# Kernel tuning notes

Hardware: AMD Instinct MI355X
Metric: run time of the kernel (lower is better)

## Reference

```python
import jax, jax.numpy as jnp
import numpy as np

N_NODES = 10000
EPS = 1e-5


def _layernorm(x, gamma, beta):
    mu = jnp.mean(x, axis=-1, keepdims=True)
    var = jnp.mean(jnp.square(x - mu), axis=-1, keepdims=True)
    return (x - mu) * jax.lax.rsqrt(var + EPS) * gamma + beta


def _sage_pool_layer(h, src, dst, Wp, bp, Ws, Wn, b, gamma, beta):
    # DGL SAGEConv(aggregator='pool'):
    #   m_u = relu(h_u @ Wp^T + bp); h_neigh[v] = max_{u in N(v)} m_u (0 if no neighbors)
    #   rst = h @ Ws^T + h_neigh @ Wn^T + b
    m = jax.nn.relu(h @ Wp.T + bp)              # [N, d]
    msg = m[src]                                 # [E, d] gather
    agg = jax.ops.segment_max(msg, dst, num_segments=N_NODES)
    agg = jnp.where(jnp.isfinite(agg), agg, 0.0)  # isolated nodes -> 0
    rst = h @ Ws.T + agg @ Wn.T + b
    # gsage_layer: LayerNorm, then Encoder applies relu (dropout inactive in eval)
    return jax.nn.relu(_layernorm(rst, gamma, beta))


def setup_inputs() -> dict:
    key = jax.random.key(0)
    ks = jax.random.split(key, 16)
    d = 256
    E = 320000
    s = 1.0 / np.sqrt(d)
    inp = {
        "h": jax.random.normal(ks[0], (N_NODES, d), dtype=jnp.float32),
        "edge_src": jax.random.randint(ks[1], (E,), 0, N_NODES, dtype=jnp.int32),
        "edge_dst": jax.random.randint(ks[2], (E,), 0, N_NODES, dtype=jnp.int32),
    }
    for li in range(2):
        kk = jax.random.split(ks[3 + li], 3)
        inp[f"Wp{li}"] = jax.random.normal(kk[0], (d, d), dtype=jnp.float32) * s
        inp[f"bp{li}"] = jnp.zeros((d,), jnp.float32)
        inp[f"Ws{li}"] = jax.random.normal(kk[1], (d, d), dtype=jnp.float32) * s
        inp[f"Wn{li}"] = jax.random.normal(kk[2], (d, d), dtype=jnp.float32) * s
        inp[f"b{li}"] = jnp.zeros((d,), jnp.float32)
        inp[f"g{li}"] = jnp.ones((d,), jnp.float32)
        inp[f"be{li}"] = jnp.zeros((d,), jnp.float32)
    return inp


def reference(h, edge_src, edge_dst,
              Wp0, bp0, Ws0, Wn0, b0, g0, be0,
              Wp1, bp1, Ws1, Wn1, b1, g1, be1):
    h = _sage_pool_layer(h, edge_src, edge_dst, Wp0, bp0, Ws0, Wn0, b0, g0, be0)
    h = _sage_pool_layer(h, edge_src, edge_dst, Wp1, bp1, Ws1, Wn1, b1, g1, be1)
    return h
```

## Files before the change

kernel.cpp:

```cpp
#include <hip/hip_runtime.h>

#define D 256
#define CAP 128
#define ASTRIDE 280
#define LN_EPS 1e-5f

typedef short short8 __attribute__((ext_vector_type(8)));
typedef float floatx4 __attribute__((ext_vector_type(4)));
typedef unsigned short u16x4 __attribute__((ext_vector_type(4)));

typedef const __attribute__((address_space(1))) void* gas_t;
typedef __attribute__((address_space(3))) void* las_t;

#define WAIT_VM(n) __builtin_amdgcn_s_waitcnt(((n) & 0xF) | (((n) >> 4) << 14) | (7 << 4) | (0xF << 8))

__device__ __forceinline__ u16x4 umax4(u16x4 a, u16x4 b) {
#if __has_builtin(__builtin_elementwise_max)
    return __builtin_elementwise_max(a, b);
#else
    u16x4 r;
    r.x = a.x > b.x ? a.x : b.x; r.y = a.y > b.y ? a.y : b.y;
    r.z = a.z > b.z ? a.z : b.z; r.w = a.w > b.w ? a.w : b.w;
    return r;
#endif
}

__device__ __forceinline__ unsigned short f2b(float f) {
    union { float f; unsigned int u; } x; x.f = f;
    unsigned int u = x.u + 0x7FFFu + ((x.u >> 16) & 1u);
    return (unsigned short)(u >> 16);
}

#define GEMM_HALF(APTR_EXPR, WPTR, K0H)                                         \
    {                                                                           \
        short8 aF[4], bF[4][4];                                                 \
        _Pragma("unroll") for (int ks = 0; ks < 4; ks++)                        \
            aF[ks] = APTR_EXPR(K0H + ks * 32);                                  \
        _Pragma("unroll") for (int ks = 0; ks < 4; ks++)                        \
        _Pragma("unroll") for (int t = 0; t < 4; t++)                           \
            bF[ks][t] = *(const short8*)((WPTR) + t * 16 * D + (K0H) + ks * 32);\
        _Pragma("unroll") for (int ks = 0; ks < 4; ks++) {                      \
            acc[0] = __builtin_amdgcn_mfma_f32_16x16x32_bf16(aF[ks], bF[ks][0], acc[0], 0, 0, 0); \
            acc[1] = __builtin_amdgcn_mfma_f32_16x16x32_bf16(aF[ks], bF[ks][1], acc[1], 0, 0, 0); \
            acc[2] = __builtin_amdgcn_mfma_f32_16x16x32_bf16(aF[ks], bF[ks][2], acc[2], 0, 0, 0); \
            acc[3] = __builtin_amdgcn_mfma_f32_16x16x32_bf16(aF[ks], bF[ks][3], acc[3], 0, 0, 0); \
        }                                                                       \
    }

__global__ __launch_bounds__(256) void prep_kernel(
    const float* __restrict__ w0, const float* __restrict__ w1,
    const float* __restrict__ w2, const float* __restrict__ w3,
    const float* __restrict__ w4, const float* __restrict__ w5,
    unsigned short* __restrict__ wb,
    const float* __restrict__ h, unsigned short* __restrict__ hb, int nh4,
    int* __restrict__ cnt, unsigned short* __restrict__ mb, int N)
{
    const int blk = blockIdx.x;
    const int tid = threadIdx.x;
    if (blk < 384) {
        const int wsel = blk >> 6;
        const float* src;
        switch (wsel) {
            case 0: src = w0; break; case 1: src = w1; break;
            case 2: src = w2; break; case 3: src = w3; break;
            case 4: src = w4; break; default: src = w5; break;
        }
        const int idx = (blk & 63) * 1024 + tid * 4;
        const float4 v = *(const float4*)(src + idx);
        ushort4 o;
        o.x = f2b(v.x); o.y = f2b(v.y); o.z = f2b(v.z); o.w = f2b(v.w);
        *(ushort4*)(wb + (size_t)wsel * 65536 + idx) = o;
    } else if (blk < 1024) {
        int i = (blk - 384) * 256 + tid;
        const int stride = 640 * 256;
        for (; i < nh4; i += stride) {
            const float4 v = *(const float4*)(h + (size_t)i * 4);
            ushort4 o;
            o.x = f2b(v.x); o.y = f2b(v.y); o.z = f2b(v.z); o.w = f2b(v.w);
            *(ushort4*)(hb + (size_t)i * 4) = o;
        }
    } else if (blk < 1064) {
        const int i = (blk - 1024) * 256 + tid;
        if (i < N) cnt[i] = 0;
    } else {
        mb[(size_t)N * D + tid] = 0;
    }
}

__global__ __launch_bounds__(64, 4) void gemm_relu(
    const unsigned short* __restrict__ A, const unsigned short* __restrict__ W,
    const float* __restrict__ bias, unsigned short* __restrict__ out_b, int N,
    const int* __restrict__ esrc, const int* __restrict__ edst,
    int* __restrict__ cnt, unsigned short* __restrict__ csr, int E, int ngemm)
{
    if ((int)blockIdx.x >= ngemm) {
        const int nsb = gridDim.x - ngemm;
        int i = ((int)blockIdx.x - ngemm) * 64 + threadIdx.x;
        const int stride = nsb * 64;
        for (; i < E; i += stride) {
            const int d = edst[i];
            const int pos = atomicAdd(&cnt[d], 1);
            if (pos < CAP) csr[(size_t)d * CAP + pos] = (unsigned short)esrc[i];
        }
        return;
    }

    const int lane = threadIdx.x;
    const int quad = lane >> 4;
    const int l16 = lane & 15;
    const int blk = blockIdx.x;
    const int row0 = (blk >> 2) * 16;
    const int col0 = (blk & 3) * 64;
    const int koff = quad * 8;

    floatx4 acc[4];
#pragma unroll
    for (int t = 0; t < 4; t++) acc[t] = (floatx4)(0.f);

    const unsigned short* aptr = A + (size_t)(row0 + l16) * D + koff;
    const unsigned short* wptr = W + (size_t)(col0 + l16) * D + koff;
#define A_GLOBAL(K) (*(const short8*)(aptr + (K)))
    GEMM_HALF(A_GLOBAL, wptr, 0)
    GEMM_HALF(A_GLOBAL, wptr, 128)
#undef A_GLOBAL

#pragma unroll
    for (int t = 0; t < 4; t++) {
        const float bcol = bias[col0 + t * 16 + l16];
#pragma unroll
        for (int r = 0; r < 4; r++) {
            const int rg = row0 + quad * 4 + r;
            const int col = col0 + t * 16 + l16;
            out_b[(size_t)rg * D + col] = f2b(fmaxf(acc[t][r] + bcol, 0.f));
        }
    }
}

__global__ __launch_bounds__(256, 3) void gemm_ln_pool(
    const unsigned short* __restrict__ A, const unsigned short* __restrict__ Wself,
    const unsigned short* __restrict__ Wneigh,
    const unsigned short* __restrict__ mpool,
    const int* __restrict__ cnt, const unsigned short* __restrict__ csr,
    const float* __restrict__ bias,
    const float* __restrict__ gamma, const float* __restrict__ beta,
    unsigned short* __restrict__ out_b, float* __restrict__ out_f, int N)
{
    __shared__ unsigned short idxS[16][CAP];
    __shared__ unsigned short gbuf[4][2][8][D];
    __shared__ unsigned short aggS[16 * ASTRIDE];
    __shared__ float redS[4][16], redS2[4][16], muA[16], rsA[16];

    const int tid = threadIdx.x;
    const int wave = tid >> 6;
    const int lane = tid & 63;
    const int quad = lane >> 4;
    const int l16 = lane & 15;
    const int row0 = blockIdx.x * 16;
    const int koff = quad * 8;
    const int rbase = wave * 4;
    const int half = lane >> 5;
    const int l32 = lane & 31;

    int degs[4];
#pragma unroll
    for (int rr = 0; rr < 4; rr++) degs[rr] = min(cnt[row0 + rbase + rr], CAP);
    int P = max(max(degs[0], degs[1]), max(degs[2], degs[3]));
    const int P2 = (P + 1) & ~1;
#pragma unroll
    for (int rr = 0; rr < 4; rr++) {
        const int rg = row0 + rbase + rr;
        for (int i = lane; i < P2; i += 64)
            idxS[rbase + rr][i] = (i < degs[rr]) ? csr[(size_t)rg * CAP + i]
                                                 : (unsigned short)N;
    }

    floatx4 acc[4];
#pragma unroll
    for (int t = 0; t < 4; t++) acc[t] = (floatx4)(0.f);

    {
        const unsigned short* aptr = A + (size_t)(row0 + l16) * D + koff;
        const unsigned short* wptr = Wself + (size_t)(wave * 64 + l16) * D + koff;
#pragma unroll
        for (int k0 = 0; k0 < D; k0 += 32) {
            const short8 av = *(const short8*)(aptr + k0);
            const short8 b0 = *(const short8*)(wptr + k0);
            const short8 b1 = *(const short8*)(wptr + 16 * D + k0);
            const short8 b2 = *(const short8*)(wptr + 32 * D + k0);
            const short8 b3 = *(const short8*)(wptr + 48 * D + k0);
            acc[0] = __builtin_amdgcn_mfma_f32_16x16x32_bf16(av, b0, acc[0], 0, 0, 0);
            acc[1] = __builtin_amdgcn_mfma_f32_16x16x32_bf16(av, b1, acc[1], 0, 0, 0);
            acc[2] = __builtin_amdgcn_mfma_f32_16x16x32_bf16(av, b2, acc[2], 0, 0, 0);
            acc[3] = __builtin_amdgcn_mfma_f32_16x16x32_bf16(av, b3, acc[3], 0, 0, 0);
        }
    }

    {
        const int nb = P2 >> 1;
        u16x4 mx[4];
#pragma unroll
        for (int rr = 0; rr < 4; rr++) mx[rr] = (u16x4)(0);

#define ISSUE_BURST(bi, buf)                                                    \
        {                                                                       \
            _Pragma("unroll") for (int rr = 0; rr < 4; rr++) {                  \
                const int jj = idxS[rbase + rr][2 * (bi) + half];               \
                const unsigned short* g = mpool + (size_t)jj * D + l32 * 8;     \
                __builtin_amdgcn_global_load_lds(                               \
                    (gas_t)g, (las_t)&gbuf[wave][buf][rr * 2][0], 16, 0, 0);    \
            }                                                                   \
        }

        if (nb > 0) ISSUE_BURST(0, 0);
        if (nb > 1) ISSUE_BURST(1, 1);
        for (int b = 0; b < nb; b++) {
            if (b + 1 < nb) WAIT_VM(4); else WAIT_VM(0);
            const int buf = b & 1;
#pragma unroll
            for (int rr = 0; rr < 4; rr++) {
                const u16x4 a0 = *(const u16x4*)&gbuf[wave][buf][rr * 2 + 0][lane * 4];
                const u16x4 a1 = *(const u16x4*)&gbuf[wave][buf][rr * 2 + 1][lane * 4];
                mx[rr] = umax4(mx[rr], umax4(a0, a1));
            }
            if (b + 2 < nb) ISSUE_BURST(b + 2, buf);
        }
#undef ISSUE_BURST
#pragma unroll
        for (int rr = 0; rr < 4; rr++)
            *(u16x4*)&aggS[(rbase + rr) * ASTRIDE + lane * 4] = mx[rr];
    }
    __syncthreads();

    {
        const unsigned short* wptr = Wneigh + (size_t)(wave * 64 + l16) * D + koff;
#pragma unroll
        for (int k0 = 0; k0 < D; k0 += 32) {
            const short8 av = *(const short8*)&aggS[l16 * ASTRIDE + koff + k0];
            const short8 b0 = *(const short8*)(wptr + k0);
            const short8 b1 = *(const short8*)(wptr + 16 * D + k0);
            const short8 b2 = *(const short8*)(wptr + 32 * D + k0);
            const short8 b3 = *(const short8*)(wptr + 48 * D + k0);
            acc[0] = __builtin_amdgcn_mfma_f32_16x16x32_bf16(av, b0, acc[0], 0, 0, 0);
            acc[1] = __builtin_amdgcn_mfma_f32_16x16x32_bf16(av, b1, acc[1], 0, 0, 0);
            acc[2] = __builtin_amdgcn_mfma_f32_16x16x32_bf16(av, b2, acc[2], 0, 0, 0);
            acc[3] = __builtin_amdgcn_mfma_f32_16x16x32_bf16(av, b3, acc[3], 0, 0, 0);
        }
    }

    float bcol[4];
#pragma unroll
    for (int t = 0; t < 4; t++) bcol[t] = bias[wave * 64 + t * 16 + l16];
#pragma unroll
    for (int t = 0; t < 4; t++)
#pragma unroll
        for (int r = 0; r < 4; r++) acc[t][r] += bcol[t];

#pragma unroll
    for (int r = 0; r < 4; r++) {
        float s = 0.f, s2 = 0.f;
#pragma unroll
        for (int t = 0; t < 4; t++) {
            const float v = acc[t][r];
            s += v; s2 += v * v;
        }
        s += __shfl_xor(s, 1);  s2 += __shfl_xor(s2, 1);
        s += __shfl_xor(s, 2);  s2 += __shfl_xor(s2, 2);
        s += __shfl_xor(s, 4);  s2 += __shfl_xor(s2, 4);
        s += __shfl_xor(s, 8);  s2 += __shfl_xor(s2, 8);
        if (l16 == 0) {
            redS[wave][quad * 4 + r] = s;
            redS2[wave][quad * 4 + r] = s2;
        }
    }
    __syncthreads();
    if (tid < 16) {
        const float S  = redS[0][tid] + redS[1][tid] + redS[2][tid] + redS[3][tid];
        const float S2 = redS2[0][tid] + redS2[1][tid] + redS2[2][tid] + redS2[3][tid];
        const float mu = S * (1.f / D);
        float var = S2 * (1.f / D) - mu * mu;
        var = fmaxf(var, 0.f);
        muA[tid] = mu;
        rsA[tid] = rsqrtf(var + LN_EPS);
    }
    __syncthreads();

    float gcol[4], becol[4];
#pragma unroll
    for (int t = 0; t < 4; t++) {
        gcol[t] = gamma[wave * 64 + t * 16 + l16];
        becol[t] = beta[wave * 64 + t * 16 + l16];
    }
#pragma unroll
    for (int r = 0; r < 4; r++) {
        const int rl = quad * 4 + r;
        const int rg = row0 + rl;
        const float mu = muA[rl];
        const float rs = rsA[rl];
#pragma unroll
        for (int t = 0; t < 4; t++) {
            const int col = wave * 64 + t * 16 + l16;
            float o = (acc[t][r] - mu) * rs * gcol[t] + becol[t];
            o = fmaxf(o, 0.f);
            if (out_f) out_f[(size_t)rg * D + col] = o;
            else       out_b[(size_t)rg * D + col] = f2b(o);
        }
    }
}

extern "C" void kernel_launch(void* const* d_in, const int* in_sizes, int n_in,
                              void* d_out, int out_size, void* d_ws, size_t ws_size,
                              hipStream_t stream) {
    const float* h    = (const float*)d_in[0];
    const int*   esrc = (const int*)d_in[1];
    const int*   edst = (const int*)d_in[2];
    const float* Wp0  = (const float*)d_in[3];
    const float* bp0  = (const float*)d_in[4];
    const float* Ws0  = (const float*)d_in[5];
    const float* Wn0  = (const float*)d_in[6];
    const float* b0   = (const float*)d_in[7];
    const float* g0   = (const float*)d_in[8];
    const float* be0  = (const float*)d_in[9];
    const float* Wp1  = (const float*)d_in[10];
    const float* bp1  = (const float*)d_in[11];
    const float* Ws1  = (const float*)d_in[12];
    const float* Wn1  = (const float*)d_in[13];
    const float* b1   = (const float*)d_in[14];
    const float* g1   = (const float*)d_in[15];
    const float* be1  = (const float*)d_in[16];

    const int N = in_sizes[0] / D;
    const int E = in_sizes[1];
    const size_t ND = (size_t)N * D;

    unsigned short* hb  = (unsigned short*)d_ws;
    unsigned short* mb  = hb + ND;
    unsigned short* h1b = mb + ND + D;
    unsigned short* wb  = h1b + ND;
    int* cnt = (int*)(wb + 6 * 65536);
    unsigned short* csr = (unsigned short*)(cnt + N);

    unsigned short* wpb0 = wb + 0 * 65536;
    unsigned short* wsb0 = wb + 1 * 65536;
    unsigned short* wnb0 = wb + 2 * 65536;
    unsigned short* wpb1 = wb + 3 * 65536;
    unsigned short* wsb1 = wb + 4 * 65536;
    unsigned short* wnb1 = wb + 5 * 65536;

    const int rblocks = (N / 16) * 4;
    const int pblocks = N / 16;
    const int sblocks = 1024;

    prep_kernel<<<1065, 256, 0, stream>>>(Wp0, Ws0, Wn0, Wp1, Ws1, Wn1, wb,
                                          h, hb, (int)(ND / 4), cnt, mb, N);

    gemm_relu<<<rblocks + sblocks, 64, 0, stream>>>(hb, wpb0, bp0, mb, N,
                                                    esrc, edst, cnt, csr, E, rblocks);
    gemm_ln_pool<<<pblocks, 256, 0, stream>>>(hb, wsb0, wnb0, mb, cnt, csr,
                                              b0, g0, be0, h1b, nullptr, N);

    gemm_relu<<<rblocks, 64, 0, stream>>>(h1b, wpb1, bp1, mb, N,
                                          esrc, edst, cnt, csr, 0, rblocks);
    gemm_ln_pool<<<pblocks, 256, 0, stream>>>(h1b, wsb1, wnb1, mb, cnt, csr,
                                              b1, g1, be1, nullptr, (float*)d_out, N);
}
```

Measured before the change: 216.1 us.

## Fuse fp32-to-bf16 input conversion into layer-0 GEMM loads and regroup row blocks

Drops the separate pass that converted the fp32 node features to bf16 in the prep kernel. The layer-0 GEMMs now read fp32 rows directly and convert them to bf16 in registers. The gemm_relu block index is also remapped so groups of 8 row tiles share their 4 column tiles, which should improve L2 reuse of A rows. This removes one full write-and-read of the feature matrix, but layer 0 now reads twice as many bytes for A in both GEMMs and adds a runtime branch on the A source.

New measurement: 217.5 us. Within noise of the previous version (+0.6%).

```diff
diff --git a/kernel.cpp b/kernel.cpp
--- a/kernel.cpp
+++ b/kernel.cpp
@@ -31,11 +31,22 @@
     return (unsigned short)(u >> 16);
 }
 
-#define GEMM_HALF(APTR_EXPR, WPTR, K0H)                                         \
+__device__ __forceinline__ short8 ldA_f32(const float* p) {
+    const float4 a = *(const float4*)p;
+    const float4 b = *(const float4*)(p + 4);
+    short8 r;
+    r[0] = (short)f2b(a.x); r[1] = (short)f2b(a.y);
+    r[2] = (short)f2b(a.z); r[3] = (short)f2b(a.w);
+    r[4] = (short)f2b(b.x); r[5] = (short)f2b(b.y);
+    r[6] = (short)f2b(b.z); r[7] = (short)f2b(b.w);
+    return r;
+}
+
+#define GEMM_HALF(A_EXPR, WPTR, K0H)                                            \
     {                                                                           \
         short8 aF[4], bF[4][4];                                                 \
         _Pragma("unroll") for (int ks = 0; ks < 4; ks++)                        \
-            aF[ks] = APTR_EXPR(K0H + ks * 32);                                  \
+            aF[ks] = A_EXPR(K0H + ks * 32);                                     \
         _Pragma("unroll") for (int ks = 0; ks < 4; ks++)                        \
         _Pragma("unroll") for (int t = 0; t < 4; t++)                           \
             bF[ks][t] = *(const short8*)((WPTR) + t * 16 * D + (K0H) + ks * 32);\
@@ -52,7 +63,6 @@
     const float* __restrict__ w2, const float* __restrict__ w3,
     const float* __restrict__ w4, const float* __restrict__ w5,
     unsigned short* __restrict__ wb,
-    const float* __restrict__ h, unsigned short* __restrict__ hb, int nh4,
     int* __restrict__ cnt, unsigned short* __restrict__ mb, int N)
 {
     const int blk = blockIdx.x;
@@ -70,17 +80,8 @@
         ushort4 o;
         o.x = f2b(v.x); o.y = f2b(v.y); o.z = f2b(v.z); o.w = f2b(v.w);
         *(ushort4*)(wb + (size_t)wsel * 65536 + idx) = o;
-    } else if (blk < 1024) {
-        int i = (blk - 384) * 256 + tid;
-        const int stride = 640 * 256;
-        for (; i < nh4; i += stride) {
-            const float4 v = *(const float4*)(h + (size_t)i * 4);
-            ushort4 o;
-            o.x = f2b(v.x); o.y = f2b(v.y); o.z = f2b(v.z); o.w = f2b(v.w);
-            *(ushort4*)(hb + (size_t)i * 4) = o;
-        }
-    } else if (blk < 1064) {
-        const int i = (blk - 1024) * 256 + tid;
+    } else if (blk < 424) {
+        const int i = (blk - 384) * 256 + tid;
         if (i < N) cnt[i] = 0;
     } else {
         mb[(size_t)N * D + tid] = 0;
@@ -88,8 +89,9 @@
 }
 
 __global__ __launch_bounds__(64, 4) void gemm_relu(
-    const unsigned short* __restrict__ A, const unsigned short* __restrict__ W,
-    const float* __restrict__ bias, unsigned short* __restrict__ out_b, int N,
+    const float* __restrict__ Af, const unsigned short* __restrict__ Ab,
+    const unsigned short* __restrict__ W,
+    const float* __restrict__ bias, unsigned short* __restrict__ out_b, int nrow,
     const int* __restrict__ esrc, const int* __restrict__ edst,
     int* __restrict__ cnt, unsigned short* __restrict__ csr, int E, int ngemm)
 {
@@ -105,39 +107,47 @@
         return;
     }
 
+    const int blk = blockIdx.x;
+    const int g = blk >> 5;
+    const int o = blk & 31;
+    const int c = o >> 3;
+    const int r = g * 8 + (o & 7);
+    if (r >= nrow) return;
+
     const int lane = threadIdx.x;
     const int quad = lane >> 4;
     const int l16 = lane & 15;
-    const int blk = blockIdx.x;
-    const int row0 = (blk >> 2) * 16;
-    const int col0 = (blk & 3) * 64;
+    const int row0 = r * 16;
+    const int col0 = c * 64;
     const int koff = quad * 8;
 
     floatx4 acc[4];
 #pragma unroll
     for (int t = 0; t < 4; t++) acc[t] = (floatx4)(0.f);
 
-    const unsigned short* aptr = A + (size_t)(row0 + l16) * D + koff;
+    const unsigned short* aptr = Ab ? Ab + (size_t)(row0 + l16) * D + koff : nullptr;
+    const float*          afp  = Af ? Af + (size_t)(row0 + l16) * D + koff : nullptr;
     const unsigned short* wptr = W + (size_t)(col0 + l16) * D + koff;
-#define A_GLOBAL(K) (*(const short8*)(aptr + (K)))
-    GEMM_HALF(A_GLOBAL, wptr, 0)
-    GEMM_HALF(A_GLOBAL, wptr, 128)
-#undef A_GLOBAL
+#define A_SRC(K) (Af ? ldA_f32(afp + (K)) : *(const short8*)(aptr + (K)))
+    GEMM_HALF(A_SRC, wptr, 0)
+    GEMM_HALF(A_SRC, wptr, 128)
+#undef A_SRC
 
 #pragma unroll
     for (int t = 0; t < 4; t++) {
         const float bcol = bias[col0 + t * 16 + l16];
 #pragma unroll
-        for (int r = 0; r < 4; r++) {
-            const int rg = row0 + quad * 4 + r;
+        for (int rr = 0; rr < 4; rr++) {
+            const int rg = row0 + quad * 4 + rr;
             const int col = col0 + t * 16 + l16;
-            out_b[(size_t)rg * D + col] = f2b(fmaxf(acc[t][r] + bcol, 0.f));
+            out_b[(size_t)rg * D + col] = f2b(fmaxf(acc[t][rr] + bcol, 0.f));
         }
     }
 }
 
 __global__ __launch_bounds__(256, 3) void gemm_ln_pool(
-    const unsigned short* __restrict__ A, const unsigned short* __restrict__ Wself,
+    const float* __restrict__ Af, const unsigned short* __restrict__ Ab,
+    const unsigned short* __restrict__ Wself,
     const unsigned short* __restrict__ Wneigh,
     const unsigned short* __restrict__ mpool,
     const int* __restrict__ cnt, const unsigned short* __restrict__ csr,
@@ -179,11 +189,12 @@
     for (int t = 0; t < 4; t++) acc[t] = (floatx4)(0.f);
 
     {
-        const unsigned short* aptr = A + (size_t)(row0 + l16) * D + koff;
+        const unsigned short* aptr = Ab ? Ab + (size_t)(row0 + l16) * D + koff : nullptr;
+        const float*          afp  = Af ? Af + (size_t)(row0 + l16) * D + koff : nullptr;
         const unsigned short* wptr = Wself + (size_t)(wave * 64 + l16) * D + koff;
 #pragma unroll
         for (int k0 = 0; k0 < D; k0 += 32) {
-            const short8 av = *(const short8*)(aptr + k0);
+            const short8 av = Af ? ldA_f32(afp + k0) : *(const short8*)(aptr + k0);
             const short8 b0 = *(const short8*)(wptr + k0);
             const short8 b1 = *(const short8*)(wptr + 16 * D + k0);
             const short8 b2 = *(const short8*)(wptr + 32 * D + k0);
@@ -205,9 +216,9 @@
         {                                                                       \
             _Pragma("unroll") for (int rr = 0; rr < 4; rr++) {                  \
                 const int jj = idxS[rbase + rr][2 * (bi) + half];               \
-                const unsigned short* g = mpool + (size_t)jj * D + l32 * 8;     \
+                const unsigned short* gp = mpool + (size_t)jj * D + l32 * 8;    \
                 __builtin_amdgcn_global_load_lds(                               \
-                    (gas_t)g, (las_t)&gbuf[wave][buf][rr * 2][0], 16, 0, 0);    \
+                    (gas_t)gp, (las_t)&gbuf[wave][buf][rr * 2][0], 16, 0, 0);   \
             }                                                                   \
         }
 
@@ -332,8 +343,7 @@
     const int E = in_sizes[1];
     const size_t ND = (size_t)N * D;
 
-    unsigned short* hb  = (unsigned short*)d_ws;
-    unsigned short* mb  = hb + ND;
+    unsigned short* mb  = (unsigned short*)d_ws;
     unsigned short* h1b = mb + ND + D;
     unsigned short* wb  = h1b + ND;
     int* cnt = (int*)(wb + 6 * 65536);
@@ -346,20 +356,21 @@
     unsigned short* wsb1 = wb + 4 * 65536;
     unsigned short* wnb1 = wb + 5 * 65536;
 
-    const int rblocks = (N / 16) * 4;
-    const int pblocks = N / 16;
+    const int nrow = N / 16;
+    const int rblocks = ((nrow + 7) / 8) * 32;
+    const int pblocks = nrow;
     const int sblocks = 1024;
 
-    prep_kernel<<<1065, 256, 0, stream>>>(Wp0, Ws0, Wn0, Wp1, Ws1, Wn1, wb,
-                                          h, hb, (int)(ND / 4), cnt, mb, N);
-
-    gemm_relu<<<rblocks + sblocks, 64, 0, stream>>>(hb, wpb0, bp0, mb, N,
+    prep_kernel<<<425, 256, 0, stream>>>(Wp0, Ws0, Wn0, Wp1, Ws1, Wn1, wb,
+                                         cnt, mb, N);
+
+    gemm_relu<<<rblocks + sblocks, 64, 0, stream>>>(h, nullptr, wpb0, bp0, mb, nrow,
                                                     esrc, edst, cnt, csr, E, rblocks);
-    gemm_ln_pool<<<pblocks, 256, 0, stream>>>(hb, wsb0, wnb0, mb, cnt, csr,
+    gemm_ln_pool<<<pblocks, 256, 0, stream>>>(h, nullptr, wsb0, wnb0, mb, cnt, csr,
                                               b0, g0, be0, h1b, nullptr, N);
 
-    gemm_relu<<<rblocks, 64, 0, stream>>>(h1b, wpb1, bp1, mb, N,
+    gemm_relu<<<rblocks, 64, 0, stream>>>(nullptr, h1b, wpb1, bp1, mb, nrow,
                                           esrc, edst, cnt, csr, 0, rblocks);
-    gemm_ln_pool<<<pblocks, 256, 0, stream>>>(h1b, wsb1, wnb1, mb, cnt, csr,
+    gemm_ln_pool<<<pblocks, 256, 0, stream>>>(nullptr, h1b, wsb1, wnb1, mb, cnt, csr,
                                               b1, g1, be1, nullptr, (float*)d_out, N);
 }
```
